# Kernel optimization log

Measured on AMD Instinct MI355X. Metric: run time of the kernel, lower is better.

Reference implementation:

```python
import jax, jax.numpy as jnp
import numpy as np

EMB_DIM = 256
N_PTS = 2048  # decoder output points
LN_EPS = 1e-5


def setup_inputs() -> dict:
    key = jax.random.key(0)
    ks = jax.random.split(key, 20)
    B, N = 16, 4096

    def w(k, shape, fan_in):
        return (jax.random.normal(k, shape, dtype=jnp.float32) / np.sqrt(fan_in)).astype(jnp.float32)

    return {
        "in_pc": jax.random.normal(ks[0], (B, N, 3), dtype=jnp.float32),
        # encoder: 1x1 convs == per-point linear over channels
        "conv1_w": w(ks[1], (64, 3), 3),     "conv1_b": jnp.zeros((64,), jnp.float32),
        "conv2_w": w(ks[2], (128, 64), 64),  "conv2_b": jnp.zeros((128,), jnp.float32),
        "conv3_w": w(ks[3], (1024, 256), 256), "conv3_b": jnp.zeros((1024,), jnp.float32),
        "fc_enc_w": w(ks[4], (EMB_DIM, 1024), 1024), "fc_enc_b": jnp.zeros((EMB_DIM,), jnp.float32),
        # decoder
        "fc1_w": w(ks[5], (512, EMB_DIM), EMB_DIM), "fc1_b": jnp.zeros((512,), jnp.float32),
        "fc2_w": w(ks[6], (1024, 512), 512),        "fc2_b": jnp.zeros((1024,), jnp.float32),
        "fc3_w": w(ks[7], (3 * N_PTS, 1024), 1024), "fc3_b": jnp.zeros((3 * N_PTS,), jnp.float32),
        "ln_g": jnp.ones((3 * N_PTS,), jnp.float32), "ln_b": jnp.zeros((3 * N_PTS,), jnp.float32),
    }


def _pointwise(x, w, b):
    # x: (B, Cin, N), w: (Cout, Cin) -> (B, Cout, N)   (Conv1d with kernel=1)
    return jnp.einsum('bcn,oc->bon', x, w) + b[None, :, None]


def _chamfer(p, q):
    # p: (B,N,3), q: (B,M,3). Squared-L2 pairwise distance + min reductions.
    p2 = jnp.sum(p * p, axis=-1)                      # (B,N)
    q2 = jnp.sum(q * q, axis=-1)                      # (B,M)
    d = p2[:, :, None] + q2[:, None, :] - 2.0 * jnp.einsum('bnd,bmd->bnm', p, q)  # (B,N,M)
    return jnp.min(d, axis=2), jnp.min(d, axis=1)     # (B,N), (B,M)


def reference(in_pc, conv1_w, conv1_b, conv2_w, conv2_b, conv3_w, conv3_b,
              fc_enc_w, fc_enc_b, fc1_w, fc1_b, fc2_w, fc2_b, fc3_w, fc3_b,
              ln_g, ln_b):
    B, N, _ = in_pc.shape
    # ---- encoder ----
    xyz = jnp.transpose(in_pc, (0, 2, 1))            # (B,3,N)
    x = jax.nn.relu(_pointwise(xyz, conv1_w, conv1_b))   # (B,64,N)
    x = jax.nn.relu(_pointwise(x, conv2_w, conv2_b))     # (B,128,N)
    gfeat = jnp.max(x, axis=2, keepdims=True)            # (B,128,1) adaptive_max_pool1d(x,1)
    x0 = jnp.concatenate([x, jnp.broadcast_to(gfeat, (B, 128, N))], axis=1)  # (B,256,N)
    x = jax.nn.relu(_pointwise(x0, conv3_w, conv3_b))    # (B,1024,N)
    x = jnp.max(x, axis=2)                               # (B,1024)
    emb = x @ fc_enc_w.T + fc_enc_b                      # (B,EMB_DIM)
    # ---- decoder ----
    h = jax.nn.relu(emb @ fc1_w.T + fc1_b)               # (B,512)
    h = jax.nn.relu(h @ fc2_w.T + fc2_b)                 # (B,1024)
    h = h @ fc3_w.T + fc3_b                              # (B,3*N_PTS)
    mu = jnp.mean(h, axis=-1, keepdims=True)
    var = jnp.mean((h - mu) ** 2, axis=-1, keepdims=True)
    h = (h - mu) * jax.lax.rsqrt(var + LN_EPS) * ln_g + ln_b
    out_pc = h.reshape(B, -1, 3)                         # (B,N_PTS,3)
    # ---- chamfer reconstruction loss ----
    d1, d2 = _chamfer(in_pc, out_pc)
    loss = jnp.mean(d1) + jnp.mean(d2)
    return (x0, emb, out_pc, loss)
```

## Files before the change

kernel.cpp:

```cpp
#include <hip/hip_runtime.h>

#define OUT_X0   0
#define OUT_EMB  16777216
#define OUT_OPC  16781312
#define OUT_LOSS 16879616

#define OFF_GFEAT 0
#define OFF_POOL  8192
#define OFF_GCON  73728
#define OFF_EMB   139264
#define OFF_HD1   155648
#define OFF_HD2   188416
#define OFF_H3    253952
#define OFF_OPC   647168
#define OFF_D1M   1040384
#define OFF_D2M   1302528
#define OFF_PS    1433600
#define OFF_W3BF  1433984
#define OFF_CNT   1958272
#define H2_BYTES  (16u*1024*1024)

typedef short short8 __attribute__((ext_vector_type(8)));
typedef float f32x4  __attribute__((ext_vector_type(4)));
typedef float f32x2  __attribute__((ext_vector_type(2)));

__device__ __forceinline__ unsigned short f2bf(float f){
  unsigned u = __float_as_uint(f);
  return (unsigned short)((u + 0x7FFFu + ((u >> 16) & 1u)) >> 16);
}

__device__ __forceinline__ f32x2 pkfma(f32x2 a, f32x2 b, f32x2 c){
  f32x2 d;
  asm("v_pk_fma_f32 %0, %1, %2, %3" : "=v"(d) : "v"(a), "v"(b), "v"(c));
  return d;
}

__global__ __launch_bounds__(256) void conv12_mfma(
    const float* __restrict__ in_pc,
    const float* __restrict__ w1, const float* __restrict__ b1,
    const float* __restrict__ w2, const float* __restrict__ b2,
    float* __restrict__ x0, unsigned short* __restrict__ h2b,
    unsigned* __restrict__ gfeatU,
    const float* __restrict__ w3, unsigned* __restrict__ w3bf,
    char* __restrict__ small)
{
  __shared__ unsigned short w2s[8192];
  __shared__ unsigned short h1s[8192];
  __shared__ float b2s[128];
  __shared__ unsigned gmax[128];
  int tid = threadIdx.x, bid = blockIdx.x;
  if (bid < 115){
    int i = bid*256 + tid;
    if (i < 4608) ((uint4*)(small + OFF_GFEAT))[i] = make_uint4(0u,0u,0u,0u);
    int j = i - 4608;
    if (j >= 0 && j < 24576)
      ((uint4*)(small + OFF_D1M))[j] =
        make_uint4(0x7F7F7F7Fu,0x7F7F7F7Fu,0x7F7F7F7Fu,0x7F7F7F7Fu);
    if (i == 29184) *(int*)(small + OFF_CNT) = 0;
    return;
  }
  if (bid >= 627){
    int i = (bid-627)*256 + tid;
    float2 v = ((const float2*)w3)[i];
    w3bf[i] = (unsigned)f2bf(v.x) | ((unsigned)f2bf(v.y)<<16);
    return;
  }
  int cb = bid - 115;
  int b = cb >> 5;
  int nt0 = (cb & 31)*128;
  for (int i = tid; i < 2048; i += 256){
    int ch = i >> 4, q = i & 15;
    float4 v = ((const float4*)w2)[i];
    unsigned lo = (unsigned)f2bf(v.x) | ((unsigned)f2bf(v.y)<<16);
    unsigned hi = (unsigned)f2bf(v.z) | ((unsigned)f2bf(v.w)<<16);
    int byte = (ch*128 + q*8) ^ ((ch&7)<<4);
    *(uint2*)((char*)w2s + byte) = make_uint2(lo, hi);
  }
  if (tid < 128){ b2s[tid] = b2[tid]; gmax[tid] = 0u; }
  {
    int pt = tid & 127;
    int qb = (tid >> 7) * 16;
    int idx = b*4096 + nt0 + pt;
    const float* p = in_pc + (size_t)idx*3;
    float px=p[0], py=p[1], pz=p[2];
    unsigned hp[16];
    #pragma unroll
    for (int q=0;q<16;q++){
      int c = (qb + q)*2;
      float v0 = fmaxf(fmaf(w1[c*3  ],px, fmaf(w1[c*3+1],py, fmaf(w1[c*3+2],pz, b1[c  ]))), 0.f);
      float v1 = fmaxf(fmaf(w1[c*3+3],px, fmaf(w1[c*3+4],py, fmaf(w1[c*3+5],pz, b1[c+1]))), 0.f);
      hp[q] = (unsigned)f2bf(v0) | ((unsigned)f2bf(v1)<<16);
    }
    #pragma unroll
    for (int t=0;t<4;t++){
      int byte = (pt*128 + qb*4 + t*16) ^ ((pt&7)<<4);
      *(uint4*)((char*)h1s + byte) = make_uint4(hp[t*4],hp[t*4+1],hp[t*4+2],hp[t*4+3]);
    }
  }
  __syncthreads();
  int lane = tid & 63, w = tid >> 6;
  int g = lane >> 4, p15 = lane & 15;
  f32x4 acc[8][2] = {};
  #pragma unroll
  for (int ks=0; ks<2; ks++){
    int kb = (ks*32 + g*8)*2;
    short8 bfr[2];
    #pragma unroll
    for (int nf=0;nf<2;nf++){
      int pt = w*32 + nf*16 + p15;
      bfr[nf] = *(const short8*)((const char*)h1s + ((pt*128 + kb) ^ ((pt&7)<<4)));
    }
    #pragma unroll
    for (int mf=0;mf<8;mf++){
      int ch = mf*16 + p15;
      short8 af = *(const short8*)((const char*)w2s + ((ch*128 + kb) ^ ((ch&7)<<4)));
      acc[mf][0] = __builtin_amdgcn_mfma_f32_16x16x32_bf16(af, bfr[0], acc[mf][0], 0,0,0);
      acc[mf][1] = __builtin_amdgcn_mfma_f32_16x16x32_bf16(af, bfr[1], acc[mf][1], 0,0,0);
    }
  }
  int n_base = nt0 + w*32;
  #pragma unroll
  for (int mf=0; mf<8; mf++){
    int ch0 = mf*16 + g*4;
    float bias[4];
    #pragma unroll
    for (int j=0;j<4;j++) bias[j] = b2s[ch0+j];
    float vm[4] = {0.f,0.f,0.f,0.f};
    #pragma unroll
    for (int nf=0; nf<2; nf++){
      int n = n_base + nf*16 + p15;
      float v[4];
      #pragma unroll
      for (int j=0;j<4;j++){
        v[j] = fmaxf(acc[mf][nf][j] + bias[j], 0.f);
        vm[j] = fmaxf(vm[j], v[j]);
        x0[((size_t)(b*256 + ch0 + j))*4096 + n] = v[j];
      }
      unsigned lo = (unsigned)f2bf(v[0]) | ((unsigned)f2bf(v[1])<<16);
      unsigned hi = (unsigned)f2bf(v[2]) | ((unsigned)f2bf(v[3])<<16);
      *(uint2*)&h2b[((size_t)(b*4096 + n))*128 + ch0] = make_uint2(lo, hi);
    }
    #pragma unroll
    for (int j=0;j<4;j++){
      float m = vm[j];
      m = fmaxf(m, __shfl_xor(m,1));
      m = fmaxf(m, __shfl_xor(m,2));
      m = fmaxf(m, __shfl_xor(m,4));
      m = fmaxf(m, __shfl_xor(m,8));
      if (p15==0) atomicMax(&gmax[ch0+j], __float_as_uint(m));
    }
  }
  __syncthreads();
  if (tid < 128) atomicMax(&gfeatU[b*128 + tid], gmax[tid]);
}

__global__ __launch_bounds__(256) void gcon_k(
    const unsigned* __restrict__ gfeatU,
    const float* __restrict__ w3, const float* __restrict__ b3,
    float* __restrict__ gcon)
{
  __shared__ float gf[2048];
  int tid = threadIdx.x, bid = blockIdx.x;
  for (int i=tid;i<2048;i+=256) gf[i] = __uint_as_float(gfeatU[i]);
  __syncthreads();
  int w = tid >> 6, lane = tid & 63;
  #pragma unroll
  for (int j=0;j<2;j++){
    int o = bid*8 + w*2 + j;
    float2 wv = *(const float2*)&w3[(size_t)o*256 + 128 + lane*2];
    float bias = b3[o];
    #pragma unroll
    for (int b=0;b<16;b++){
      float v = gf[b*128 + lane*2]*wv.x + gf[b*128 + lane*2 + 1]*wv.y;
      #pragma unroll
      for (int off=32; off; off>>=1) v += __shfl_xor(v, off);
      if (lane==0) gcon[b*1024+o] = bias + v;
    }
  }
}

__global__ __launch_bounds__(512) void conv3_bcast(
    const unsigned short* __restrict__ h2b, const unsigned short* __restrict__ w3b,
    const float* __restrict__ gcon, unsigned* __restrict__ pooled,
    const unsigned* __restrict__ gfeatU, float* __restrict__ x0)
{
  __shared__ unsigned short Al[128*128];
  __shared__ unsigned short Bl[128*128];
  int tid = threadIdx.x, bid = blockIdx.x;
  if (bid >= 512){
    unsigned U = (unsigned)(bid-512)*512 + tid;
    int n4 = U & 1023, c = (U >> 10) & 127, b = U >> 17;
    float g = __uint_as_float(gfeatU[b*128+c]);
    float4 v = {g,g,g,g};
    ((float4*)x0)[(((size_t)b*256 + 128 + c)*4096)/4 + n4] = v;
    return;
  }
  int mt = bid & 31, b = bid >> 5;
  {
    const uint4* src = (const uint4*)(h2b + ((size_t)b*4096 + mt*128)*128);
    #pragma unroll
    for (int i=0;i<4;i++){
      int idx = i*512 + tid;
      int r = idx>>4, kc = idx&15;
      uint4 v = src[idx];
      int byte = (r*256 + kc*16) ^ ((r&7)<<4);
      *(uint4*)((char*)Al + byte) = v;
    }
  }
  int lane = tid & 63, wid = tid >> 6;
  int wm = wid >> 2, wn = wid & 3;
  int mbase = wm*64, nbase = wn*32;
  for (int nt=0; nt<8; nt++){
    if (nt) __syncthreads();
    {
      #pragma unroll
      for (int i=0;i<4;i++){
        int idx = i*512 + tid;
        int c = idx>>4, kc = idx&15;
        uint4 v = *(const uint4*)(w3b + ((size_t)(nt*128+c)*256 + kc*8));
        int byte = (c*256 + kc*16) ^ ((c&7)<<4);
        *(uint4*)((char*)Bl + byte) = v;
      }
    }
    __syncthreads();
    f32x4 acc[4][2] = {};
    #pragma unroll
    for (int ks=0;ks<4;ks++){
      int kb = (ks*32 + (lane>>4)*8)*2;
      short8 af[4], bfr[2];
      #pragma unroll
      for (int mi=0;mi<4;mi++){
        int row = mbase + mi*16 + (lane&15);
        af[mi] = *(const short8*)((const char*)Al + ((row*256 + kb) ^ ((row&7)<<4)));
      }
      #pragma unroll
      for (int ni=0;ni<2;ni++){
        int col = nbase + ni*16 + (lane&15);
        bfr[ni] = *(const short8*)((const char*)Bl + ((col*256 + kb) ^ ((col&7)<<4)));
      }
      #pragma unroll
      for (int mi=0;mi<4;mi++){
        #pragma unroll
        for (int ni=0;ni<2;ni++)
          acc[mi][ni] = __builtin_amdgcn_mfma_f32_16x16x32_bf16(af[mi], bfr[ni], acc[mi][ni], 0,0,0);
      }
    }
    #pragma unroll
    for (int ni=0;ni<2;ni++){
      int o = nt*128 + nbase + ni*16 + (lane&15);
      float g = gcon[b*1024 + o];
      float m = 0.f;
      #pragma unroll
      for (int mi=0;mi<4;mi++){
        f32x4 a = acc[mi][ni];
        #pragma unroll
        for (int r=0;r<4;r++){ float v = a[r]+g; m = fmaxf(m, v); }
      }
      m = fmaxf(m, 0.f);
      m = fmaxf(m, __shfl_xor(m, 16));
      m = fmaxf(m, __shfl_xor(m, 32));
      if (lane < 16) atomicMax(&pooled[(size_t)b*1024+o], __float_as_uint(m));
    }
  }
}

__global__ __launch_bounds__(256) void conv12_f32(
    const float* __restrict__ in_pc,
    const float* __restrict__ w1, const float* __restrict__ b1,
    const float* __restrict__ w2, const float* __restrict__ b2,
    float* __restrict__ x0, unsigned* __restrict__ gfeatU)
{
  __shared__ unsigned gmax[32];
  int tid = threadIdx.x;
  if (tid < 32) gmax[tid] = 0u;
  __syncthreads();
  int idx = blockIdx.x*256 + tid;
  int b = idx >> 12, n = idx & 4095;
  int gy = blockIdx.y;
  int lane = tid & 63;
  const float* p = in_pc + (size_t)idx*3;
  float px=p[0], py=p[1], pz=p[2];
  float h1[64];
  #pragma unroll
  for (int c=0;c<64;c++)
    h1[c] = fmaxf(w1[c*3]*px + w1[c*3+1]*py + w1[c*3+2]*pz + b1[c], 0.f);
  #pragma unroll
  for (int j=0;j<32;j++){
    int o = gy*32 + j;
    float a = b2[o];
    #pragma unroll
    for (int c=0;c<64;c++) a += w2[o*64+c]*h1[c];
    a = fmaxf(a, 0.f);
    x0[((size_t)b*256 + o)*4096 + n] = a;
    float m = a;
    #pragma unroll
    for (int off=32; off; off>>=1) m = fmaxf(m, __shfl_xor(m, off));
    if (lane==0) atomicMax(&gmax[j], __float_as_uint(m));
  }
  __syncthreads();
  if (tid < 32) atomicMax(&gfeatU[b*128 + gy*32 + tid], gmax[tid]);
}

__global__ __launch_bounds__(256) void bcast_gcon(
    const unsigned* __restrict__ gfeatU, float* __restrict__ x0,
    const float* __restrict__ w3, const float* __restrict__ b3,
    float* __restrict__ gcon)
{
  __shared__ float gf[2048];
  int tid = threadIdx.x;
  if (blockIdx.x < 8192){
    unsigned U = blockIdx.x*256 + tid;
    int n4 = U & 1023, c = (U >> 10) & 127, b = U >> 17;
    float g = __uint_as_float(gfeatU[b*128+c]);
    float4 v = {g,g,g,g};
    ((float4*)x0)[(((size_t)b*256 + 128 + c)*4096)/4 + n4] = v;
  } else {
    for (int i=tid;i<2048;i+=256) gf[i] = __uint_as_float(gfeatU[i]);
    __syncthreads();
    int o = (blockIdx.x - 8192)*256 + tid;
    float bias = b3[o];
    float acc[16];
    #pragma unroll
    for (int b=0;b<16;b++) acc[b]=bias;
    for (int c=0;c<128;c++){
      float wv = w3[(size_t)o*256 + 128 + c];
      #pragma unroll
      for (int b=0;b<16;b++) acc[b] += gf[b*128+c]*wv;
    }
    #pragma unroll
    for (int b=0;b<16;b++) gcon[b*1024+o] = acc[b];
  }
}

__global__ __launch_bounds__(256) void conv3n(
    const float* __restrict__ x0, const unsigned* __restrict__ gfeatU,
    const float* __restrict__ w3, const float* __restrict__ b3,
    unsigned* __restrict__ pooled)
{
  __shared__ float wrow[8][256];
  int b = blockIdx.x >> 7, og = (blockIdx.x & 127)*8, tid = threadIdx.x;
  for (int i=tid;i<2048;i+=256){ int j=i>>8, c=i&255; wrow[j][c]=w3[(size_t)(og+j)*256+c]; }
  __syncthreads();
  float gconst[8];
  #pragma unroll
  for (int j=0;j<8;j++){
    float g = b3[og+j];
    for (int c=0;c<128;c++) g += __uint_as_float(gfeatU[b*128+c])*wrow[j][128+c];
    gconst[j] = g;
  }
  const float* xb = x0 + (size_t)b*256*4096;
  float m[8];
  #pragma unroll
  for (int j=0;j<8;j++) m[j]=0.f;
  for (int n=tid;n<4096;n+=256){
    float v[8];
    #pragma unroll
    for (int j=0;j<8;j++) v[j]=gconst[j];
    for (int c=0;c<128;c++){
      float xv = xb[(size_t)c*4096 + n];
      #pragma unroll
      for (int j=0;j<8;j++) v[j] += xv*wrow[j][c];
    }
    #pragma unroll
    for (int j=0;j<8;j++) m[j] = fmaxf(m[j], v[j]);
  }
  #pragma unroll
  for (int j=0;j<8;j++){
    float v = m[j];
    for (int off=32; off; off>>=1) v = fmaxf(v, __shfl_xor(v, off));
    if ((tid&63)==0) atomicMax(&pooled[(size_t)b*1024+og+j], __float_as_uint(v));
  }
}

template<bool RELU>
__global__ __launch_bounds__(256) void fc_wave16(
    const float* __restrict__ A, const float* __restrict__ W,
    const float* __restrict__ bias, float* __restrict__ out,
    float* __restrict__ out2, int K, int O)
{
  int lane = threadIdx.x & 63, w = threadIdx.x >> 6;
  int o = blockIdx.x*4 + w;
  const float* Wr = W + (size_t)o*K;
  float acc[16];
  #pragma unroll
  for (int b=0;b<16;b++) acc[b]=0.f;
  for (int k = lane*4; k < K; k += 256){
    float4 wv = *(const float4*)&Wr[k];
    #pragma unroll
    for (int b=0;b<16;b++){
      float4 av = *(const float4*)&A[(size_t)b*K + k];
      acc[b] += wv.x*av.x + wv.y*av.y + wv.z*av.z + wv.w*av.w;
    }
  }
  #pragma unroll
  for (int b=0;b<16;b++){
    float v = acc[b];
    #pragma unroll
    for (int off=32; off; off>>=1) v += __shfl_xor(v, off);
    if (lane==0){
      v += bias[o];
      if (RELU) v = fmaxf(v, 0.f);
      out[(size_t)b*O+o] = v;
      if (out2) out2[(size_t)b*O+o] = v;
    }
  }
}

__global__ __launch_bounds__(256) void lnorm(
    const float* __restrict__ h3, const float* __restrict__ g,
    const float* __restrict__ be, float* __restrict__ outf,
    float* __restrict__ outb)
{
  int b = blockIdx.x, tid = threadIdx.x;
  const float* x = h3 + b*6144;
  float s=0.f, s2=0.f;
  for (int i=tid;i<6144;i+=256){ float v=x[i]; s+=v; s2+=v*v; }
  for (int off=32; off; off>>=1){ s += __shfl_xor(s,off); s2 += __shfl_xor(s2,off); }
  __shared__ float red[8];
  int lane = tid&63, wid = tid>>6;
  if (lane==0){ red[wid]=s; red[4+wid]=s2; }
  __syncthreads();
  s  = red[0]+red[1]+red[2]+red[3];
  s2 = red[4]+red[5]+red[6]+red[7];
  float mu  = s * (1.f/6144.f);
  float var = s2 * (1.f/6144.f) - mu*mu;
  float inv = rsqrtf(var + 1e-5f);
  for (int i=tid;i<6144;i+=256){
    float v = (x[i]-mu)*inv*g[i] + be[i];
    outf[b*6144+i] = v;
    outb[b*6144+i] = v;
  }
}

__global__ __launch_bounds__(256) void chamfer_all(
    const float* __restrict__ in_pc, const float* __restrict__ opc,
    unsigned* __restrict__ d1m, unsigned* __restrict__ d2m)
{
  __shared__ float sX[512], sY[512], sZ[512], sQ[512];
  int bid = blockIdx.x, tid = threadIdx.x;
  const float* stage;
  const float* qry;
  unsigned* outp;
  if (bid < 1024){
    int xt = bid & 15, b = (bid >> 4) & 15, mt = bid >> 8;
    stage = opc + b*6144 + mt*1536;
    qry   = in_pc + ((size_t)b*4096 + xt*256 + tid)*3;
    outp  = d1m + b*4096 + xt*256 + tid;
  } else {
    int r = bid - 1024;
    int xt = r & 7, b = (r >> 3) & 15, nt = r >> 7;
    stage = in_pc + ((size_t)b*4096 + nt*512)*3;
    qry   = opc + b*6144 + (xt*256 + tid)*3;
    outp  = d2m + b*2048 + xt*256 + tid;
  }
  for (int s = tid; s < 512; s += 256){
    const float* S = stage + s*3;
    float x=S[0], y=S[1], z=S[2];
    sX[s]=-2.f*x; sY[s]=-2.f*y; sZ[s]=-2.f*z; sQ[s]=x*x+y*y+z*z;
  }
  __syncthreads();
  float qx=qry[0], qy=qry[1], qz=qry[2];
  float p2 = qx*qx + qy*qy + qz*qz;
  f32x2 qxv = {qx,qx}, qyv = {qy,qy}, qzv = {qz,qz};
  float ma=3.0e38f, mb=3.0e38f, mc=3.0e38f, md=3.0e38f;
  #pragma unroll 4
  for (int i=0;i<128;i++){
    f32x4 X = *(const f32x4*)&sX[i*4];
    f32x4 Y = *(const f32x4*)&sY[i*4];
    f32x4 Z = *(const f32x4*)&sZ[i*4];
    f32x4 Q = *(const f32x4*)&sQ[i*4];
    f32x2 t0 = __builtin_shufflevector(Q,Q,0,1);
    f32x2 t1 = __builtin_shufflevector(Q,Q,2,3);
    t0 = pkfma(qzv, __builtin_shufflevector(Z,Z,0,1), t0);
    t1 = pkfma(qzv, __builtin_shufflevector(Z,Z,2,3), t1);
    t0 = pkfma(qyv, __builtin_shufflevector(Y,Y,0,1), t0);
    t1 = pkfma(qyv, __builtin_shufflevector(Y,Y,2,3), t1);
    t0 = pkfma(qxv, __builtin_shufflevector(X,X,0,1), t0);
    t1 = pkfma(qxv, __builtin_shufflevector(X,X,2,3), t1);
    ma = fminf(ma, t0.x); mb = fminf(mb, t0.y);
    mc = fminf(mc, t1.x); md = fminf(md, t1.y);
  }
  float d = fmaxf(p2 + fminf(fminf(ma,mb), fminf(mc,md)), 0.f);
  atomicMin(outp, __float_as_uint(d));
}

__global__ __launch_bounds__(256) void sum_loss(
    const unsigned* __restrict__ d1m, const unsigned* __restrict__ d2m,
    float* __restrict__ ps, int* __restrict__ cnt, float* __restrict__ out)
{
  int bid = blockIdx.x, tid = threadIdx.x;
  __shared__ float red[4];
  __shared__ int last;
  {
    const unsigned* src = (bid<64) ? (d1m + bid*1024) : (d2m + (size_t)(bid-64)*1024);
    float s = 0.f;
    for (int i=tid;i<1024;i+=256) s += __uint_as_float(src[i]);
    for (int off=32; off; off>>=1) s += __shfl_xor(s,off);
    if ((tid&63)==0) red[tid>>6]=s;
    __syncthreads();
    if (tid==0){
      ps[bid] = red[0]+red[1]+red[2]+red[3];
      __threadfence();
      last = (atomicAdd(cnt, 1) == 95);
    }
    __syncthreads();
  }
  if (!last) return;
  __threadfence();
  float v = 0.f;
  if (tid < 64) v = ps[tid] * (1.0f/65536.0f);
  else if (tid < 96) v = ps[tid] * (1.0f/32768.0f);
  for (int off=32; off; off>>=1) v += __shfl_xor(v,off);
  __syncthreads();
  if ((tid&63)==0) red[tid>>6]=v;
  __syncthreads();
  if (tid==0) out[0] = red[0]+red[1]+red[2]+red[3];
}

extern "C" void kernel_launch(void* const* d_in, const int* in_sizes, int n_in,
                              void* d_out, int out_size, void* d_ws, size_t ws_size,
                              hipStream_t stream)
{
  (void)in_sizes; (void)n_in; (void)out_size;
  const float* in_pc = (const float*)d_in[0];
  const float* w1   = (const float*)d_in[1];
  const float* b1   = (const float*)d_in[2];
  const float* w2   = (const float*)d_in[3];
  const float* b2   = (const float*)d_in[4];
  const float* w3   = (const float*)d_in[5];
  const float* b3   = (const float*)d_in[6];
  const float* wenc = (const float*)d_in[7];
  const float* benc = (const float*)d_in[8];
  const float* wf1  = (const float*)d_in[9];
  const float* bfc1 = (const float*)d_in[10];
  const float* wf2  = (const float*)d_in[11];
  const float* bfc2 = (const float*)d_in[12];
  const float* wf3  = (const float*)d_in[13];
  const float* bfc3 = (const float*)d_in[14];
  const float* lng  = (const float*)d_in[15];
  const float* lnb  = (const float*)d_in[16];
  float* out = (float*)d_out;

  bool big = ws_size >= (size_t)(H2_BYTES + 3*1024*1024);
  char* ws = (char*)d_ws;
  unsigned short* h2b = (unsigned short*)ws;
  char* small = ws + (big ? H2_BYTES : 0);

  unsigned* gfeatU = (unsigned*)(small + OFF_GFEAT);
  float* pooled = (float*)(small + OFF_POOL);
  float* gcon = (float*)(small + OFF_GCON);
  float* emb  = (float*)(small + OFF_EMB);
  float* hd1  = (float*)(small + OFF_HD1);
  float* hd2  = (float*)(small + OFF_HD2);
  float* h3   = (float*)(small + OFF_H3);
  float* opc  = (float*)(small + OFF_OPC);
  unsigned* d1m = (unsigned*)(small + OFF_D1M);
  unsigned* d2m = (unsigned*)(small + OFF_D2M);
  float* ps   = (float*)(small + OFF_PS);
  unsigned short* w3b = (unsigned short*)(small + OFF_W3BF);
  int* cnt = (int*)(small + OFF_CNT);

  if (big){
    conv12_mfma<<<1139, 256, 0, stream>>>(in_pc, w1, b1, w2, b2, out, h2b, gfeatU,
                                          w3, (unsigned*)w3b, small);
    gcon_k<<<128, 256, 0, stream>>>(gfeatU, w3, b3, gcon);
    conv3_bcast<<<4608, 512, 0, stream>>>(h2b, w3b, gcon, (unsigned*)pooled,
                                          gfeatU, out);
  } else {
    hipMemsetAsync(small + OFF_GFEAT, 0, 8192 + 65536, stream);
    hipMemsetAsync(small + OFF_D1M, 0x7F, 262144 + 131072, stream);
    hipMemsetAsync(small + OFF_CNT, 0, 4, stream);
    conv12_f32<<<dim3(256,4), 256, 0, stream>>>(in_pc, w1, b1, w2, b2, out, gfeatU);
    bcast_gcon<<<8196, 256, 0, stream>>>(gfeatU, out, w3, b3, gcon);
    conv3n<<<2048, 256, 0, stream>>>(out, gfeatU, w3, b3, (unsigned*)pooled);
  }
  fc_wave16<false><<<64,   256, 0, stream>>>(pooled, wenc, benc, emb, out + OUT_EMB, 1024, 256);
  fc_wave16<true ><<<128,  256, 0, stream>>>(emb, wf1, bfc1, hd1, nullptr, 256, 512);
  fc_wave16<true ><<<256,  256, 0, stream>>>(hd1, wf2, bfc2, hd2, nullptr, 512, 1024);
  fc_wave16<false><<<1536, 256, 0, stream>>>(hd2, wf3, bfc3, h3, nullptr, 1024, 6144);
  lnorm<<<16, 256, 0, stream>>>(h3, lng, lnb, opc, out + OUT_OPC);
  chamfer_all<<<2048, 256, 0, stream>>>(in_pc, opc, d1m, d2m);
  sum_loss<<<96, 256, 0, stream>>>(d1m, d2m, ps, cnt, out + OUT_LOSS);
}
```

Measured before the change: 155.9 us.

## Fuse decoder FC chain and layernorm into one persistent kernel with grid barriers

Replaces the five decoder launches (four FC layers plus layernorm) on the main path with a single 256-block kernel that steps through the layers and separates them with a global atomic-counter barrier. A second counter is zeroed by the init blocks. The aim is to remove launch gaps and tail idle time between the tiny dependent GEMVs. In exchange, the last FC layer runs with only 256 blocks doing 6 outputs per wave, which lowers parallelism, and the spin barrier relies on all 256 blocks being co-resident.

```diff
diff --git a/kernel.cpp b/kernel.cpp
--- a/kernel.cpp
+++ b/kernel.cpp
@@ -18,6 +18,7 @@
 #define OFF_PS    1433600
 #define OFF_W3BF  1433984
 #define OFF_CNT   1958272
+#define OFF_CNT2  1958276
 #define H2_BYTES  (16u*1024*1024)
 
 typedef short short8 __attribute__((ext_vector_type(8)));
@@ -57,6 +58,7 @@
       ((uint4*)(small + OFF_D1M))[j] =
         make_uint4(0x7F7F7F7Fu,0x7F7F7F7Fu,0x7F7F7F7Fu,0x7F7F7F7Fu);
     if (i == 29184) *(int*)(small + OFF_CNT) = 0;
+    if (i == 29185) *(int*)(small + OFF_CNT2) = 0;
     return;
   }
   if (bid >= 627){
@@ -261,6 +263,99 @@
       m = fmaxf(m, __shfl_xor(m, 32));
       if (lane < 16) atomicMax(&pooled[(size_t)b*1024+o], __float_as_uint(m));
     }
+  }
+}
+
+__device__ __forceinline__ void fc16_dot(
+    const float* __restrict__ A, const float* __restrict__ Wr, float bias,
+    bool relu, float* __restrict__ out, float* __restrict__ out2,
+    int K, int O, int o, int lane)
+{
+  float acc[16];
+  #pragma unroll
+  for (int b=0;b<16;b++) acc[b]=0.f;
+  for (int k = lane*4; k < K; k += 256){
+    float4 wv = *(const float4*)&Wr[k];
+    #pragma unroll
+    for (int b=0;b<16;b++){
+      float4 av = *(const float4*)&A[(size_t)b*K + k];
+      acc[b] += wv.x*av.x + wv.y*av.y + wv.z*av.z + wv.w*av.w;
+    }
+  }
+  #pragma unroll
+  for (int b=0;b<16;b++){
+    float v = acc[b];
+    #pragma unroll
+    for (int off=32; off; off>>=1) v += __shfl_xor(v, off);
+    if (lane==0){
+      v += bias;
+      if (relu) v = fmaxf(v, 0.f);
+      out[(size_t)b*O+o] = v;
+      if (out2) out2[(size_t)b*O+o] = v;
+    }
+  }
+}
+
+__device__ __forceinline__ void gsync(int* c, int target){
+  __syncthreads();
+  if (threadIdx.x==0){
+    __threadfence();
+    atomicAdd(c, 1);
+    while (atomicAdd(c, 0) < target) __builtin_amdgcn_s_sleep(8);
+  }
+  __syncthreads();
+}
+
+__global__ __launch_bounds__(256) void decoder_k(
+    const float* __restrict__ pooled,
+    const float* __restrict__ wenc, const float* __restrict__ benc,
+    const float* __restrict__ wf1, const float* __restrict__ bfc1,
+    const float* __restrict__ wf2, const float* __restrict__ bfc2,
+    const float* __restrict__ wf3, const float* __restrict__ bfc3,
+    const float* __restrict__ lng, const float* __restrict__ lnb,
+    float* __restrict__ emb, float* __restrict__ hd1, float* __restrict__ hd2,
+    float* __restrict__ h3, float* __restrict__ opc,
+    float* __restrict__ outbuf, int* __restrict__ cnt2)
+{
+  int tid = threadIdx.x, lane = tid & 63;
+  int gw = blockIdx.x*4 + (tid >> 6);
+  if (gw < 256)
+    fc16_dot(pooled, wenc + (size_t)gw*1024, benc[gw], false,
+             emb, outbuf + OUT_EMB, 1024, 256, gw, lane);
+  gsync(cnt2, 256);
+  if (gw < 512)
+    fc16_dot(emb, wf1 + (size_t)gw*256, bfc1[gw], true,
+             hd1, nullptr, 256, 512, gw, lane);
+  gsync(cnt2, 512);
+  fc16_dot(hd1, wf2 + (size_t)gw*512, bfc2[gw], true,
+           hd2, nullptr, 512, 1024, gw, lane);
+  gsync(cnt2, 768);
+  #pragma unroll
+  for (int j=0;j<6;j++){
+    int o = gw*6 + j;
+    fc16_dot(hd2, wf3 + (size_t)o*1024, bfc3[o], false,
+             h3, nullptr, 1024, 6144, o, lane);
+  }
+  gsync(cnt2, 1024);
+  int b = blockIdx.x;
+  if (b >= 16) return;
+  const float* x = h3 + b*6144;
+  float s=0.f, s2=0.f;
+  for (int i=tid;i<6144;i+=256){ float v=x[i]; s+=v; s2+=v*v; }
+  for (int off=32; off; off>>=1){ s += __shfl_xor(s,off); s2 += __shfl_xor(s2,off); }
+  __shared__ float red[8];
+  int wid = tid>>6;
+  if (lane==0){ red[wid]=s; red[4+wid]=s2; }
+  __syncthreads();
+  s  = red[0]+red[1]+red[2]+red[3];
+  s2 = red[4]+red[5]+red[6]+red[7];
+  float mu  = s * (1.f/6144.f);
+  float var = s2 * (1.f/6144.f) - mu*mu;
+  float inv = rsqrtf(var + 1e-5f);
+  for (int i=tid;i<6144;i+=256){
+    float v = (x[i]-mu)*inv*lng[i] + lnb[i];
+    opc[b*6144+i] = v;
+    outbuf[OUT_OPC + b*6144+i] = v;
   }
 }
 
@@ -380,30 +475,7 @@
 {
   int lane = threadIdx.x & 63, w = threadIdx.x >> 6;
   int o = blockIdx.x*4 + w;
-  const float* Wr = W + (size_t)o*K;
-  float acc[16];
-  #pragma unroll
-  for (int b=0;b<16;b++) acc[b]=0.f;
-  for (int k = lane*4; k < K; k += 256){
-    float4 wv = *(const float4*)&Wr[k];
-    #pragma unroll
-    for (int b=0;b<16;b++){
-      float4 av = *(const float4*)&A[(size_t)b*K + k];
-      acc[b] += wv.x*av.x + wv.y*av.y + wv.z*av.z + wv.w*av.w;
-    }
-  }
-  #pragma unroll
-  for (int b=0;b<16;b++){
-    float v = acc[b];
-    #pragma unroll
-    for (int off=32; off; off>>=1) v += __shfl_xor(v, off);
-    if (lane==0){
-      v += bias[o];
-      if (RELU) v = fmaxf(v, 0.f);
-      out[(size_t)b*O+o] = v;
-      if (out2) out2[(size_t)b*O+o] = v;
-    }
-  }
+  fc16_dot(A, W + (size_t)o*K, bias[o], RELU, out, out2, K, O, o, lane);
 }
 
 __global__ __launch_bounds__(256) void lnorm(
@@ -559,6 +631,7 @@
   float* ps   = (float*)(small + OFF_PS);
   unsigned short* w3b = (unsigned short*)(small + OFF_W3BF);
   int* cnt = (int*)(small + OFF_CNT);
+  int* cnt2 = (int*)(small + OFF_CNT2);
 
   if (big){
     conv12_mfma<<<1139, 256, 0, stream>>>(in_pc, w1, b1, w2, b2, out, h2b, gfeatU,
@@ -566,19 +639,22 @@
     gcon_k<<<128, 256, 0, stream>>>(gfeatU, w3, b3, gcon);
     conv3_bcast<<<4608, 512, 0, stream>>>(h2b, w3b, gcon, (unsigned*)pooled,
                                           gfeatU, out);
+    decoder_k<<<256, 256, 0, stream>>>(pooled, wenc, benc, wf1, bfc1, wf2, bfc2,
+                                       wf3, bfc3, lng, lnb, emb, hd1, hd2, h3,
+                                       opc, out, cnt2);
   } else {
     hipMemsetAsync(small + OFF_GFEAT, 0, 8192 + 65536, stream);
     hipMemsetAsync(small + OFF_D1M, 0x7F, 262144 + 131072, stream);
-    hipMemsetAsync(small + OFF_CNT, 0, 4, stream);
+    hipMemsetAsync(small + OFF_CNT, 0, 8, stream);
     conv12_f32<<<dim3(256,4), 256, 0, stream>>>(in_pc, w1, b1, w2, b2, out, gfeatU);
     bcast_gcon<<<8196, 256, 0, stream>>>(gfeatU, out, w3, b3, gcon);
     conv3n<<<2048, 256, 0, stream>>>(out, gfeatU, w3, b3, (unsigned*)pooled);
-  }
-  fc_wave16<false><<<64,   256, 0, stream>>>(pooled, wenc, benc, emb, out + OUT_EMB, 1024, 256);
-  fc_wave16<true ><<<128,  256, 0, stream>>>(emb, wf1, bfc1, hd1, nullptr, 256, 512);
-  fc_wave16<true ><<<256,  256, 0, stream>>>(hd1, wf2, bfc2, hd2, nullptr, 512, 1024);
-  fc_wave16<false><<<1536, 256, 0, stream>>>(hd2, wf3, bfc3, h3, nullptr, 1024, 6144);
-  lnorm<<<16, 256, 0, stream>>>(h3, lng, lnb, opc, out + OUT_OPC);
+    fc_wave16<false><<<64,   256, 0, stream>>>(pooled, wenc, benc, emb, out + OUT_EMB, 1024, 256);
+    fc_wave16<true ><<<128,  256, 0, stream>>>(emb, wf1, bfc1, hd1, nullptr, 256, 512);
+    fc_wave16<true ><<<256,  256, 0, stream>>>(hd1, wf2, bfc2, hd2, nullptr, 512, 1024);
+    fc_wave16<false><<<1536, 256, 0, stream>>>(hd2, wf3, bfc3, h3, nullptr, 1024, 6144);
+    lnorm<<<16, 256, 0, stream>>>(h3, lng, lnb, opc, out + OUT_OPC);
+  }
   chamfer_all<<<2048, 256, 0, stream>>>(in_pc, opc, d1m, d2m);
   sum_loss<<<96, 256, 0, stream>>>(d1m, d2m, ps, cnt, out + OUT_LOSS);
 }
```

New measurement: 203.0 us. 30.2% more time.
